# Kernel optimization log

Hardware: AMD Instinct MI355X
Metric: run time of the kernel (lower is better)

The kernel has to match this reference:

```python
import jax, jax.numpy as jnp
import numpy as np

N_NODES = 200000
N_GRAPHS = 1024
BN_EPS = 1e-5


def setup_inputs() -> dict:
    key = jax.random.key(0)
    ks = jax.random.split(key, 24)
    s = 0.05
    inp = {
        "x": jax.random.normal(ks[0], (N_NODES, 78), jnp.float32),
        "edge_index": jax.random.randint(ks[1], (2, 3200000), 0, N_NODES, jnp.int32),
        "batch": jnp.sort(jax.random.randint(ks[2], (N_NODES,), 0, N_GRAPHS, jnp.int32)),
        "target": jax.random.randint(ks[3], (N_GRAPHS, 1000), 0, 26, jnp.int32),
        "g1_w1": jax.random.normal(ks[4], (78, 32), jnp.float32) * s,
        "g1_b1": jnp.zeros((32,), jnp.float32),
        "g1_w2": jax.random.normal(ks[5], (32, 32), jnp.float32) * s,
        "g1_b2": jnp.zeros((32,), jnp.float32),
        "gW1": jax.random.normal(ks[6], (4, 32, 32), jnp.float32) * s,
        "gb1": jnp.zeros((4, 32), jnp.float32),
        "gW2": jax.random.normal(ks[7], (4, 32, 32), jnp.float32) * s,
        "gb2": jnp.zeros((4, 32), jnp.float32),
        "bn_gamma": jnp.ones((5, 32), jnp.float32),
        "bn_beta": jnp.zeros((5, 32), jnp.float32),
        "fcxd_w": jax.random.normal(ks[8], (32, 128), jnp.float32) * s,
        "fcxd_b": jnp.zeros((128,), jnp.float32),
        "embed_xt": jax.random.normal(ks[9], (26, 128), jnp.float32) * s,
        "conv_w": jax.random.normal(ks[10], (32, 1000, 8), jnp.float32) * 0.01,
        "conv_b": jnp.zeros((32,), jnp.float32),
        "fcxt_w": jax.random.normal(ks[11], (3872, 128), jnp.float32) * 0.01,
        "fcxt_b": jnp.zeros((128,), jnp.float32),
        "fc1_w": jax.random.normal(ks[12], (256, 1024), jnp.float32) * s,
        "fc1_b": jnp.zeros((1024,), jnp.float32),
        "fc2_w": jax.random.normal(ks[13], (1024, 256), jnp.float32) * s,
        "fc2_b": jnp.zeros((256,), jnp.float32),
        "out_w": jax.random.normal(ks[14], (256, 1), jnp.float32) * s,
        "out_b": jnp.zeros((1,), jnp.float32),
    }
    return inp


def _gin_layer(h, edge_index, W1, b1, W2, b2, gamma, beta):
    # GINConv (eps=0): mlp(x + sum_{j in N(i)} x_j), then ReLU then BatchNorm
    agg = jax.ops.segment_sum(h[edge_index[0]], edge_index[1], num_segments=N_NODES)
    z = h + agg
    z = jnp.maximum(z @ W1 + b1, 0.0) @ W2 + b2
    z = jnp.maximum(z, 0.0)
    mu = z.mean(axis=0)
    var = z.var(axis=0)
    return (z - mu) * jax.lax.rsqrt(var + BN_EPS) * gamma + beta


def reference(x, edge_index, batch, target,
              g1_w1, g1_b1, g1_w2, g1_b2,
              gW1, gb1, gW2, gb2, bn_gamma, bn_beta,
              fcxd_w, fcxd_b, embed_xt, conv_w, conv_b,
              fcxt_w, fcxt_b, fc1_w, fc1_b, fc2_w, fc2_b, out_w, out_b):
    # --- molecule GIN branch (dropout = identity at inference) ---
    h = _gin_layer(x, edge_index, g1_w1, g1_b1, g1_w2, g1_b2, bn_gamma[0], bn_beta[0])
    for i in range(4):
        h = _gin_layer(h, edge_index, gW1[i], gb1[i], gW2[i], gb2[i],
                       bn_gamma[i + 1], bn_beta[i + 1])
    # global add pool over graphs
    pooled = jax.ops.segment_sum(h, batch, num_segments=N_GRAPHS)  # [B,32]
    xd = jnp.maximum(pooled @ fcxd_w + fcxd_b, 0.0)                # [B,128]

    # --- protein branch: embed -> Conv1d(in_ch=seq_len=1000, k=8) -> linear ---
    e = embed_xt[target]                                            # [B,1000,128]
    conv = jax.lax.conv_general_dilated(
        e, conv_w, window_strides=(1,), padding='VALID',
        dimension_numbers=('NCH', 'OIH', 'NCH'))                    # [B,32,121]
    conv = conv + conv_b[None, :, None]
    xt = conv.reshape(conv.shape[0], -1) @ fcxt_w + fcxt_b          # [B,128]

    # --- combined dense head ---
    xc = jnp.concatenate([xd, xt], axis=1)                          # [B,256]
    xc = jnp.maximum(xc @ fc1_w + fc1_b, 0.0)
    xc = xc @ fc2_w + fc2_b
    return xc @ out_w + out_b                                       # [B,1]
```

## Files before the change

kernel.cpp:

```cpp
#include <hip/hip_runtime.h>
#include <hip/hip_fp16.h>

#define HID 32
#define BN_EPS 1e-5f
#define NBMAX 512
#define BSHIFT 9
#define SCAT_CH 8192
#define FSTRIDE 10240
#define FCAP 10240
#define DP_CH 4096

static __device__ __forceinline__ int lbound(const int* a, int n, int key) {
    int lo = 0, hi = n;
    while (lo < hi) { int m = (lo + hi) >> 1; if (a[m] < key) lo = m + 1; else hi = m; }
    return lo;
}

static __device__ __forceinline__ unsigned packh2(float a, float b) {
    __half2 h = __floats2half2_rn(a, b);
    return *reinterpret_cast<unsigned*>(&h);
}
static __device__ __forceinline__ float lo_h(unsigned v) {
    __half2 h = *reinterpret_cast<__half2*>(&v);
    return __low2float(h);
}
static __device__ __forceinline__ float hi_h(unsigned v) {
    __half2 h = *reinterpret_cast<__half2*>(&v);
    return __high2float(h);
}
static __device__ __forceinline__ float h2f(unsigned short v) {
    return __half2float(__ushort_as_half(v));
}

static __device__ __forceinline__ void addu4h(float* a, uint4 v) {
    a[0] += lo_h(v.x); a[1] += hi_h(v.x);
    a[2] += lo_h(v.y); a[3] += hi_h(v.y);
    a[4] += lo_h(v.z); a[5] += hi_h(v.z);
    a[6] += lo_h(v.w); a[7] += hi_h(v.w);
}

__global__ void __launch_bounds__(256) k_bscatter(const int* __restrict__ ei,
                                                  int* __restrict__ gcur,
                                                  int* __restrict__ pairs, int E, int NB) {
    __shared__ int h[NBMAX];
    __shared__ int lb[NBMAX];
    int t = threadIdx.x;
    int c0 = blockIdx.x * SCAT_CH;
    int end = min(c0 + SCAT_CH, E);
    for (int i = t; i < NBMAX; i += 256) h[i] = 0;
    __syncthreads();
    for (int i = c0 + t; i < end; i += 256)
        atomicAdd(&h[ei[E + i] >> BSHIFT], 1);
    __syncthreads();
    for (int b = t; b < NB; b += 256) {
        int c = h[b];
        lb[b] = c ? atomicAdd(&gcur[b], c) : 0;
        h[b] = 0;
    }
    __syncthreads();
    for (int i = c0 + t; i < end; i += 256) {
        int src = ei[i], d = ei[E + i];
        int bkt = d >> BSHIFT;
        int r = atomicAdd(&h[bkt], 1);
        pairs[bkt * FSTRIDE + lb[bkt] + r] = src | ((d & 511) << 18);
    }
}

__global__ void __launch_bounds__(512) k_bscan(const int* __restrict__ gcur,
                                               int* __restrict__ bbase,
                                               int* __restrict__ rowstart,
                                               int N, int E, int NB) {
    __shared__ int s[512];
    int t = threadIdx.x;
    int v = (t < NB) ? gcur[t] : 0;
    s[t] = v; __syncthreads();
    for (int off = 1; off < 512; off <<= 1) {
        int u = (t >= off) ? s[t - off] : 0; __syncthreads();
        s[t] += u; __syncthreads();
    }
    int excl = s[t] - v;
    if (t < NB) bbase[t] = excl;
    if (t == NB - 1) bbase[NB] = s[t];
    if (t == 0) rowstart[N] = E;
}

__global__ void __launch_bounds__(512) k_bfinal(const int* __restrict__ pairs,
                                                const int* __restrict__ bbase,
                                                const int* __restrict__ gcur,
                                                int* __restrict__ rowstart,
                                                int* __restrict__ csr, int N) {
    __shared__ int h[2048];
    __shared__ int ts[512];
    __shared__ int loc[FCAP];
    int t = threadIdx.x;
    int b = blockIdx.x;
    int base = bbase[b];
    int cnt = gcur[b];
    const int* bp = pairs + (size_t)b * FSTRIDE;
    for (int i = t; i < 2048; i += 512) h[i] = 0;
    __syncthreads();
    for (int i = t; i < cnt; i += 512) {
        int p = bp[i];
        int key = ((p >> 18) << 2) | ((p & 0x3ffff) >> 16);
        atomicAdd(&h[key], 1);
    }
    __syncthreads();
    int v0 = h[4 * t], v1 = h[4 * t + 1], v2 = h[4 * t + 2], v3 = h[4 * t + 3];
    int lsum = v0 + v1 + v2 + v3;
    ts[t] = lsum; __syncthreads();
    for (int off = 1; off < 512; off <<= 1) {
        int u = (t >= off) ? ts[t - off] : 0; __syncthreads();
        ts[t] += u; __syncthreads();
    }
    int texcl = ts[t] - lsum;
    h[4 * t]     = texcl;
    h[4 * t + 1] = texcl + v0;
    h[4 * t + 2] = texcl + v0 + v1;
    h[4 * t + 3] = texcl + v0 + v1 + v2;
    int node = b * 512 + t;
    if (node < N) rowstart[node] = base + texcl;
    __syncthreads();
    bool fit = (cnt <= FCAP);
    for (int i = t; i < cnt; i += 512) {
        int p = bp[i];
        int key = ((p >> 18) << 2) | ((p & 0x3ffff) >> 16);
        int r = atomicAdd(&h[key], 1);
        int src = p & 0x3ffff;
        if (fit) loc[r] = src; else csr[base + r] = src;
    }
    __syncthreads();
    if (fit)
        for (int i = t; i < cnt; i += 512) csr[base + i] = loc[i];
}

__global__ void __launch_bounds__(256) k_dhist(const int* __restrict__ rowstart,
                                               int* __restrict__ dh, int N) {
    __shared__ int h[512];
    int t = threadIdx.x;
    for (int i = t; i < 512; i += 256) h[i] = 0;
    __syncthreads();
    for (int i = blockIdx.x * 256 + t; i < N; i += gridDim.x * 256) {
        int d = min(rowstart[i + 1] - rowstart[i], 511);
        atomicAdd(&h[d], 1);
    }
    __syncthreads();
    for (int i = t; i < 512; i += 256)
        if (h[i]) atomicAdd(&dh[i], h[i]);
}

__global__ void __launch_bounds__(512) k_dscan(const int* __restrict__ dh,
                                               int* __restrict__ dcur) {
    __shared__ int s[512];
    int t = threadIdx.x;
    int v = dh[511 - t];
    s[t] = v; __syncthreads();
    for (int off = 1; off < 512; off <<= 1) {
        int u = (t >= off) ? s[t - off] : 0; __syncthreads();
        s[t] += u; __syncthreads();
    }
    dcur[511 - t] = s[t] - v;
}

__global__ void __launch_bounds__(256) k_dplace2(const int* __restrict__ rowstart,
                                                 int* __restrict__ dcur,
                                                 int* __restrict__ perm, int N) {
    __shared__ int h[512];
    __shared__ int base[512];
    int t = threadIdx.x;
    int c0 = blockIdx.x * DP_CH;
    int end = min(c0 + DP_CH, N);
    for (int i = t; i < 512; i += 256) h[i] = 0;
    __syncthreads();
    for (int i = c0 + t; i < end; i += 256) {
        int d = min(rowstart[i + 1] - rowstart[i], 511);
        atomicAdd(&h[d], 1);
    }
    __syncthreads();
    for (int i = t; i < 512; i += 256) {
        int c = h[i];
        base[i] = c ? atomicAdd(&dcur[i], c) : 0;
        h[i] = 0;
    }
    __syncthreads();
    for (int i = c0 + t; i < end; i += 256) {
        int d = min(rowstart[i + 1] - rowstart[i], 511);
        int r = atomicAdd(&h[d], 1);
        perm[base[d] + r] = i;
    }
}

__global__ void __launch_bounds__(256) k_A1(const float* __restrict__ x,
                                            const float* __restrict__ W,
                                            unsigned* __restrict__ Ub, int N) {
    __shared__ float xl[64 * 79];
    __shared__ float wl[78 * 33];
    int t = threadIdx.x;
    int n0 = blockIdx.x * 64;
    for (int idx = t; idx < 78 * 32; idx += 256)
        wl[(idx >> 5) * 33 + (idx & 31)] = W[idx];
    long base = (long)n0 * 78;
    for (int idx = t; idx < 64 * 78; idx += 256) {
        long g = base + idx;
        xl[(idx / 78) * 79 + (idx % 78)] = (g < (long)N * 78) ? x[g] : 0.f;
    }
    __syncthreads();
    int jp = t & 15, rg = t >> 4;
    for (int rep = 0; rep < 4; rep++) {
        int n = rg + 16 * rep;
        int node = n0 + n;
        if (node >= N) break;
        float a0 = 0.f, a1 = 0.f;
        #pragma unroll
        for (int k = 0; k < 78; k++) {
            float xv = xl[n * 79 + k];
            a0 += xv * wl[k * 33 + 2 * jp];
            a1 += xv * wl[k * 33 + 2 * jp + 1];
        }
        Ub[(size_t)node * 16 + jp] = packh2(a0, a1);
    }
}

__global__ void __launch_bounds__(256) k_BCS0(const uint4* __restrict__ Ub4,
                                              const int* __restrict__ rowstart,
                                              const int* __restrict__ csr,
                                              const int* __restrict__ perm,
                                              const float* __restrict__ b1,
                                              const float* __restrict__ W2,
                                              const float* __restrict__ b2,
                                              unsigned* __restrict__ Outb,
                                              float* __restrict__ slot, int N) {
    __shared__ float w2s[32 * 33];
    __shared__ float tl[64 * 33];
    __shared__ float redS[8][33];
    __shared__ float redQ[8][33];
    __shared__ int pl[64];
    int t = threadIdx.x;
    for (int idx = t; idx < 1024; idx += 256)
        w2s[(idx >> 5) * 33 + (idx & 31)] = W2[idx];
    if (t < 64) {
        int gid = blockIdx.x * 64 + t;
        pl[t] = (gid < N) ? perm[gid] : -1;
    }
    __syncthreads();

    int g = t >> 2, l = t & 3;
    int node = pl[g];
    bool act = (node >= 0);
    int s0 = 0, s1 = 0;
    if (act) { s0 = rowstart[node]; s1 = rowstart[node + 1]; }
    float a[8] = {0.f, 0.f, 0.f, 0.f, 0.f, 0.f, 0.f, 0.f};
    if (act) addu4h(a, Ub4[(size_t)node * 4 + l]);
    int e = s0;
    for (; e + 3 < s1; e += 4) {
        int sa = csr[e], sb = csr[e + 1], sc = csr[e + 2], sd = csr[e + 3];
        uint4 va = Ub4[(size_t)sa * 4 + l];
        uint4 vb = Ub4[(size_t)sb * 4 + l];
        uint4 vc = Ub4[(size_t)sc * 4 + l];
        uint4 vd = Ub4[(size_t)sd * 4 + l];
        addu4h(a, va); addu4h(a, vb); addu4h(a, vc); addu4h(a, vd);
    }
    for (; e < s1; e++) addu4h(a, Ub4[(size_t)csr[e] * 4 + l]);
    int f0 = 8 * l;
    #pragma unroll
    for (int i = 0; i < 8; i++)
        tl[g * 33 + f0 + i] = fmaxf(a[i] + b1[f0 + i], 0.f);
    __syncthreads();

    int j = t & 31, rg2 = t >> 5;
    float ps = 0.f, pq = 0.f;
    for (int rep = 0; rep < 8; rep++) {
        int n = rg2 + 8 * rep;
        float acc = b2[j];
        #pragma unroll
        for (int k = 0; k < 32; k++) acc += tl[n * 33 + k] * w2s[k * 33 + j];
        float xv = fmaxf(acc, 0.f);
        tl[n * 33 + j] = xv;
        if (pl[n] >= 0) { ps += xv; pq += xv * xv; }
    }
    redS[rg2][j] = ps; redQ[rg2][j] = pq;
    __syncthreads();
    if (t < 32) {
        float s = 0.f, q = 0.f;
        #pragma unroll
        for (int r = 0; r < 8; r++) { s += redS[r][t]; q += redQ[r][t]; }
        int rep = blockIdx.x & 7;
        atomicAdd(&slot[rep * 64 + t], s);
        atomicAdd(&slot[rep * 64 + 32 + t], q);
    }
    for (int idx = t; idx < 1024; idx += 256) {
        int n = idx >> 4, jp = idx & 15;
        int nod = pl[n];
        if (nod >= 0)
            Outb[(size_t)nod * 16 + jp] = packh2(tl[n * 33 + 2 * jp], tl[n * 33 + 2 * jp + 1]);
    }
}

__global__ void __launch_bounds__(256) k_BCS1(const uint4* __restrict__ Xb4,
                                              const int* __restrict__ rowstart,
                                              const int* __restrict__ csr,
                                              const int* __restrict__ perm,
                                              const float* __restrict__ pslot,
                                              const float* __restrict__ pgam,
                                              const float* __restrict__ pbet,
                                              const float* __restrict__ W1,
                                              const float* __restrict__ b1,
                                              const float* __restrict__ W2,
                                              const float* __restrict__ b2,
                                              unsigned* __restrict__ Outb,
                                              float* __restrict__ slot, int N) {
    __shared__ float w1s[32 * 33];
    __shared__ float w2s[32 * 33];
    __shared__ float zl[64 * 33];
    __shared__ float aa[32], cc[32], cw[32];
    __shared__ float dp1[64];
    __shared__ float redS[8][33];
    __shared__ float redQ[8][33];
    __shared__ int pl[64];
    int t = threadIdx.x;
    if (t < 32) {
        float s = 0.f, q = 0.f;
        #pragma unroll
        for (int r = 0; r < 8; r++) { s += pslot[r * 64 + t]; q += pslot[r * 64 + 32 + t]; }
        float mu = s / (float)N;
        float var = q / (float)N - mu * mu;
        float av = pgam[t] * rsqrtf(var + BN_EPS);
        aa[t] = av;
        cc[t] = pbet[t] - mu * av;
    }
    if (t >= 64 && t < 128) {
        int gid = blockIdx.x * 64 + (t - 64);
        pl[t - 64] = (gid < N) ? perm[gid] : -1;
    }
    __syncthreads();
    for (int idx = t; idx < 1024; idx += 256) {
        int k = idx >> 5, j = idx & 31;
        w1s[k * 33 + j] = aa[k] * W1[idx];
        w2s[k * 33 + j] = W2[idx];
    }
    if (t < 32) {
        float acc = 0.f;
        for (int k = 0; k < 32; k++) acc += cc[k] * W1[k * 32 + t];
        cw[t] = acc;
    }

    int g = t >> 2, l = t & 3;
    int node = pl[g];
    bool act = (node >= 0);
    int s0 = 0, s1 = 0;
    if (act) { s0 = rowstart[node]; s1 = rowstart[node + 1]; }
    float a[8] = {0.f, 0.f, 0.f, 0.f, 0.f, 0.f, 0.f, 0.f};
    if (act) addu4h(a, Xb4[(size_t)node * 4 + l]);
    int e = s0;
    for (; e + 3 < s1; e += 4) {
        int sa = csr[e], sb = csr[e + 1], sc = csr[e + 2], sd = csr[e + 3];
        uint4 va = Xb4[(size_t)sa * 4 + l];
        uint4 vb = Xb4[(size_t)sb * 4 + l];
        uint4 vc = Xb4[(size_t)sc * 4 + l];
        uint4 vd = Xb4[(size_t)sd * 4 + l];
        addu4h(a, va); addu4h(a, vb); addu4h(a, vc); addu4h(a, vd);
    }
    for (; e < s1; e++) addu4h(a, Xb4[(size_t)csr[e] * 4 + l]);
    int f0 = 8 * l;
    #pragma unroll
    for (int i = 0; i < 8; i++) zl[g * 33 + f0 + i] = a[i];
    if (l == 0) dp1[g] = (float)(s1 - s0 + 1);
    __syncthreads();

    int j = t & 31, rg2 = t >> 5;
    float ps = 0.f, pq = 0.f;
    for (int rep = 0; rep < 8; rep++) {
        int n = rg2 + 8 * rep;
        float acc = dp1[n] * cw[j] + b1[j];
        #pragma unroll
        for (int k = 0; k < 32; k++) acc += zl[n * 33 + k] * w1s[k * 33 + j];
        zl[n * 33 + j] = fmaxf(acc, 0.f);
        float o = b2[j];
        #pragma unroll
        for (int k = 0; k < 32; k++) o += zl[n * 33 + k] * w2s[k * 33 + j];
        float xv = fmaxf(o, 0.f);
        zl[n * 33 + j] = xv;
        if (pl[n] >= 0) { ps += xv; pq += xv * xv; }
    }
    redS[rg2][j] = ps; redQ[rg2][j] = pq;
    __syncthreads();
    if (t < 32) {
        float s = 0.f, q = 0.f;
        #pragma unroll
        for (int r = 0; r < 8; r++) { s += redS[r][t]; q += redQ[r][t]; }
        int rep = blockIdx.x & 7;
        atomicAdd(&slot[rep * 64 + t], s);
        atomicAdd(&slot[rep * 64 + 32 + t], q);
    }
    for (int idx = t; idx < 1024; idx += 256) {
        int n = idx >> 4, jp = idx & 15;
        int nod = pl[n];
        if (nod >= 0)
            Outb[(size_t)nod * 16 + jp] = packh2(zl[n * 33 + 2 * jp], zl[n * 33 + 2 * jp + 1]);
    }
}

__global__ void __launch_bounds__(128) k_pool(const unsigned short* __restrict__ Xb,
                                              const int* __restrict__ batch,
                                              const float* __restrict__ pslot,
                                              const float* __restrict__ pgam,
                                              const float* __restrict__ pbet,
                                              const float* __restrict__ fw,
                                              const float* __restrict__ fb,
                                              float* __restrict__ xc, int N) {
    __shared__ float red[4][32];
    __shared__ float pv[32];
    __shared__ float aa[32], cc[32];
    int g = blockIdx.x, t = threadIdx.x;
    if (t < 32) {
        float s = 0.f, q = 0.f;
        #pragma unroll
        for (int r = 0; r < 8; r++) { s += pslot[r * 64 + t]; q += pslot[r * 64 + 32 + t]; }
        float mu = s / (float)N;
        float var = q / (float)N - mu * mu;
        float av = pgam[t] * rsqrtf(var + BN_EPS);
        aa[t] = av;
        cc[t] = pbet[t] - mu * av;
    }
    int lo = lbound(batch, N, g);
    int hi = lbound(batch, N, g + 1);
    int j = t & 31, rs = t >> 5;
    float ps = 0.f;
    for (int i = lo + rs; i < hi; i += 4) ps += h2f(Xb[(size_t)i * 32 + j]);
    red[rs][j] = ps; __syncthreads();
    if (t < 32) {
        float s = red[0][t] + red[1][t] + red[2][t] + red[3][t];
        pv[t] = s * aa[t] + (float)(hi - lo) * cc[t];
    }
    __syncthreads();
    float acc = fb[t];
    for (int k = 0; k < 32; k++) acc += pv[k] * fw[k * 128 + t];
    xc[g * 256 + t] = fmaxf(acc, 0.f);
}

__global__ void __launch_bounds__(128) k_F2(const float* __restrict__ Emb,
                                            const float* __restrict__ fcxt,
                                            float* __restrict__ F) {
    __shared__ float er[128];
    int bid = blockIdx.x;
    int v = bid >> 5, o = bid & 31;
    int t = threadIdx.x;
    er[t] = Emb[v * 128 + t];
    __syncthreads();
    float acc[8] = {0.f, 0.f, 0.f, 0.f, 0.f, 0.f, 0.f, 0.f};
    for (int p = 0; p < 121; p++) {
        float fv = fcxt[(o * 121 + p) * 128 + t];
        #pragma unroll
        for (int k = 0; k < 8; k++) acc[k] += er[p + k] * fv;
    }
    #pragma unroll
    for (int k = 0; k < 8; k++)
        F[((size_t)v * 256 + o * 8 + k) * 128 + t] = acc[k];
}

__global__ void __launch_bounds__(128) k_cb(const float* __restrict__ fcxt,
                                            const float* __restrict__ fb,
                                            const float* __restrict__ cb,
                                            float* __restrict__ cbias) {
    int o = blockIdx.x, t = threadIdx.x;
    float acc = 0.f;
    for (int p = 0; p < 121; p++) acc += fcxt[(o * 121 + p) * 128 + t];
    float val = cb[o] * acc;
    if (o == 0) val += fb[t];
    atomicAdd(&cbias[t], val);
}

__global__ void __launch_bounds__(256) k_D2(const float* __restrict__ cw,
                                            const float* __restrict__ F,
                                            unsigned* __restrict__ Dmb) {
    __shared__ float Fl[32][128];
    __shared__ float Wl[32][64];
    int v = blockIdx.y;
    int c0 = blockIdx.x * 64;
    int t = threadIdx.x;
    int jg = t & 31, j0 = jg * 4;
    int cg = t >> 5;
    float4 acc[8];
    #pragma unroll
    for (int i = 0; i < 8; i++) acc[i] = make_float4(0.f, 0.f, 0.f, 0.f);
    for (int chunk = 0; chunk < 8; chunk++) {
        int k0 = chunk * 32;
        __syncthreads();
        for (int idx = t; idx < 4096; idx += 256) {
            int k = idx >> 7, j = idx & 127;
            Fl[k][j] = F[((size_t)v * 256 + k0 + k) * 128 + j];
        }
        for (int idx = t; idx < 2048; idx += 256) {
            int k = idx >> 6, c = idx & 63;
            int ok = k0 + k;
            Wl[k][c] = (c0 + c < 1000) ? cw[((ok >> 3) * 1000 + c0 + c) * 8 + (ok & 7)] : 0.f;
        }
        __syncthreads();
        for (int k = 0; k < 32; k++) {
            float4 fv = *(const float4*)&Fl[k][j0];
            #pragma unroll
            for (int ci = 0; ci < 8; ci++) {
                float wv = Wl[k][cg * 8 + ci];
                acc[ci].x += wv * fv.x;
                acc[ci].y += wv * fv.y;
                acc[ci].z += wv * fv.z;
                acc[ci].w += wv * fv.w;
            }
        }
    }
    #pragma unroll
    for (int ci = 0; ci < 8; ci++) {
        int c = c0 + cg * 8 + ci;
        if (c < 1000) {
            uint2 pk;
            pk.x = packh2(acc[ci].x, acc[ci].y);
            pk.y = packh2(acc[ci].z, acc[ci].w);
            *(uint2*)&Dmb[((size_t)c * 26 + v) * 64 + jg * 2] = pk;
        }
    }
}

__global__ void __launch_bounds__(256) k_xt3(const int* __restrict__ target,
                                             const uint4* __restrict__ Dm4,
                                             const float* __restrict__ cbias,
                                             float* __restrict__ xc) {
    __shared__ int tl[1000];
    __shared__ float red[16][132];
    int b = blockIdx.x, t = threadIdx.x;
    for (int i = t; i < 1000; i += 256) tl[i] = target[(size_t)b * 1000 + i];
    __syncthreads();
    int cl = t >> 4;
    int jg = t & 15;
    float acc[8] = {0.f, 0.f, 0.f, 0.f, 0.f, 0.f, 0.f, 0.f};
    for (int c = cl; c < 1000; c += 16) {
        int v = tl[c];
        uint4 d = Dm4[((size_t)c * 26 + v) * 16 + jg];
        acc[0] += lo_h(d.x); acc[1] += hi_h(d.x);
        acc[2] += lo_h(d.y); acc[3] += hi_h(d.y);
        acc[4] += lo_h(d.z); acc[5] += hi_h(d.z);
        acc[6] += lo_h(d.w); acc[7] += hi_h(d.w);
    }
    #pragma unroll
    for (int fi = 0; fi < 8; fi++) red[cl][jg * 8 + fi] = acc[fi];
    __syncthreads();
    if (t < 128) {
        float s = 0.f;
        #pragma unroll
        for (int r = 0; r < 16; r++) s += red[r][t];
        xc[(size_t)b * 256 + 128 + t] = cbias[t] + s;
    }
}

__global__ void __launch_bounds__(256) k_fc1(const float* __restrict__ xc,
                                             const float* __restrict__ w,
                                             const float* __restrict__ bias,
                                             float* __restrict__ y1) {
    __shared__ float xl[16 * 256];
    int t = threadIdx.x;
    int q0 = blockIdx.x * 256, b0 = blockIdx.y * 16;
    for (int idx = t; idx < 4096; idx += 256) xl[idx] = xc[b0 * 256 + idx];
    __syncthreads();
    int ql = t & 63, q = q0 + ql * 4;
    int bg = t >> 6;
    float4 bv = *(const float4*)&bias[q];
    float4 acc0 = bv, acc1 = bv, acc2 = bv, acc3 = bv;
    const float* xr = &xl[bg * 4 * 256];
    #pragma unroll 4
    for (int k = 0; k < 256; k++) {
        float4 wv = *(const float4*)&w[k * 1024 + q];
        float x0 = xr[k], x1 = xr[256 + k], x2 = xr[512 + k], x3 = xr[768 + k];
        acc0.x += x0 * wv.x; acc0.y += x0 * wv.y; acc0.z += x0 * wv.z; acc0.w += x0 * wv.w;
        acc1.x += x1 * wv.x; acc1.y += x1 * wv.y; acc1.z += x1 * wv.z; acc1.w += x1 * wv.w;
        acc2.x += x2 * wv.x; acc2.y += x2 * wv.y; acc2.z += x2 * wv.z; acc2.w += x2 * wv.w;
        acc3.x += x3 * wv.x; acc3.y += x3 * wv.y; acc3.z += x3 * wv.z; acc3.w += x3 * wv.w;
    }
    int b = b0 + bg * 4;
    float4 r;
    r.x = fmaxf(acc0.x, 0.f); r.y = fmaxf(acc0.y, 0.f); r.z = fmaxf(acc0.z, 0.f); r.w = fmaxf(acc0.w, 0.f);
    *(float4*)&y1[(size_t)b * 1024 + q] = r;
    r.x = fmaxf(acc1.x, 0.f); r.y = fmaxf(acc1.y, 0.f); r.z = fmaxf(acc1.z, 0.f); r.w = fmaxf(acc1.w, 0.f);
    *(float4*)&y1[(size_t)(b + 1) * 1024 + q] = r;
    r.x = fmaxf(acc2.x, 0.f); r.y = fmaxf(acc2.y, 0.f); r.z = fmaxf(acc2.z, 0.f); r.w = fmaxf(acc2.w, 0.f);
    *(float4*)&y1[(size_t)(b + 2) * 1024 + q] = r;
    r.x = fmaxf(acc3.x, 0.f); r.y = fmaxf(acc3.y, 0.f); r.z = fmaxf(acc3.z, 0.f); r.w = fmaxf(acc3.w, 0.f);
    *(float4*)&y1[(size_t)(b + 3) * 1024 + q] = r;
}

__global__ void k_wcomb(const float* __restrict__ fc2w, const float* __restrict__ fc2b,
                        const float* __restrict__ ow, const float* __restrict__ ob,
                        float* __restrict__ wc) {
    int p = blockIdx.x * 256 + threadIdx.x;
    float acc = 0.f;
    for (int q = 0; q < 256; q++) acc += fc2w[p * 256 + q] * ow[q];
    wc[p] = acc;
    if (p == 0) {
        float bc = ob[0];
        for (int q = 0; q < 256; q++) bc += fc2b[q] * ow[q];
        wc[1024] = bc;
    }
}

__global__ void __launch_bounds__(256) k_out(const float* __restrict__ y1,
                                             const float* __restrict__ wc,
                                             float* __restrict__ out) {
    __shared__ float r[256];
    int b = blockIdx.x, t = threadIdx.x;
    float acc = 0.f;
    for (int p = t; p < 1024; p += 256) acc += y1[b * 1024 + p] * wc[p];
    r[t] = acc; __syncthreads();
    for (int off = 128; off > 0; off >>= 1) {
        if (t < off) r[t] += r[t + off];
        __syncthreads();
    }
    if (t == 0) out[b] = r[0] + wc[1024];
}

extern "C" void kernel_launch(void* const* d_in, const int* in_sizes, int n_in,
                              void* d_out, int out_size, void* d_ws, size_t ws_size,
                              hipStream_t stream) {
    const float* x     = (const float*)d_in[0];
    const int*   ei    = (const int*)d_in[1];
    const int*   batch = (const int*)d_in[2];
    const int*   targ  = (const int*)d_in[3];
    const float* g1w1  = (const float*)d_in[4];
    const float* g1b1  = (const float*)d_in[5];
    const float* g1w2  = (const float*)d_in[6];
    const float* g1b2  = (const float*)d_in[7];
    const float* gW1   = (const float*)d_in[8];
    const float* gb1   = (const float*)d_in[9];
    const float* gW2   = (const float*)d_in[10];
    const float* gb2   = (const float*)d_in[11];
    const float* gam   = (const float*)d_in[12];
    const float* bet   = (const float*)d_in[13];
    const float* fcxdw = (const float*)d_in[14];
    const float* fcxdb = (const float*)d_in[15];
    const float* emb   = (const float*)d_in[16];
    const float* convw = (const float*)d_in[17];
    const float* convb = (const float*)d_in[18];
    const float* fcxtw = (const float*)d_in[19];
    const float* fcxtb = (const float*)d_in[20];
    const float* fc1w  = (const float*)d_in[21];
    const float* fc1b  = (const float*)d_in[22];
    const float* fc2w  = (const float*)d_in[23];
    const float* fc2b  = (const float*)d_in[24];
    const float* outw  = (const float*)d_in[25];
    const float* outb  = (const float*)d_in[26];

    int N = in_sizes[2];
    int E = in_sizes[1] / 2;
    int B = in_sizes[3] / 1000;
    int NB = (N + 511) >> BSHIFT;

    char* ws = (char*)d_ws;
    size_t off = 0;
    auto alloc = [&](size_t bytes) -> void* {
        void* p = ws + off;
        off += (bytes + 255) & ~(size_t)255;
        return p;
    };
    int*   rowstart = (int*)alloc((size_t)(N + 1) * 4);
    int*   bbase    = (int*)alloc((NBMAX + 1) * 4);
    int*   gcur     = (int*)alloc(NBMAX * 4);
    int*   csr      = (int*)alloc((size_t)E * 4);
    int*   perm     = (int*)alloc((size_t)N * 4);
    int*   dh       = (int*)alloc(512 * 4);
    int*   dcur     = (int*)alloc(512 * 4);
    size_t xb_bytes = (size_t)N * 64;
    size_t pairs_bytes = (size_t)NB * FSTRIDE * 4;
    char*  blk      = (char*)alloc(2 * xb_bytes > pairs_bytes ? 2 * xb_bytes : pairs_bytes);
    unsigned* XbA   = (unsigned*)blk;
    unsigned* XbB   = (unsigned*)(blk + xb_bytes);
    int*   pairs    = (int*)blk;
    unsigned* Ub    = (unsigned*)alloc((size_t)N * 16 * 4);
    float* stats    = (float*)alloc((size_t)5 * 640 * 4);
    float* xc       = (float*)alloc((size_t)B * 256 * 4);
    float* Fb       = (float*)alloc((size_t)26 * 256 * 128 * 4);
    unsigned* Dmb   = (unsigned*)alloc((size_t)1000 * 26 * 64 * 4);
    float* cbias    = (float*)alloc(128 * 4);
    float* y1       = (float*)alloc((size_t)B * 1024 * 4);
    float* wc       = (float*)alloc(1025 * 4);

    hipMemsetAsync(gcur, 0, NBMAX * 4, stream);
    hipMemsetAsync(dh, 0, 512 * 4, stream);
    hipMemsetAsync(stats, 0, (size_t)5 * 640 * 4, stream);
    hipMemsetAsync(cbias, 0, 128 * 4, stream);

    k_bscatter<<<(E + SCAT_CH - 1) / SCAT_CH, 256, 0, stream>>>(ei, gcur, pairs, E, NB);
    k_bscan<<<1, 512, 0, stream>>>(gcur, bbase, rowstart, N, E, NB);
    k_bfinal<<<NB, 512, 0, stream>>>(pairs, bbase, gcur, rowstart, csr, N);

    k_dhist<<<256, 256, 0, stream>>>(rowstart, dh, N);
    k_dscan<<<1, 512, 0, stream>>>(dh, dcur);
    k_dplace2<<<(N + DP_CH - 1) / DP_CH, 256, 0, stream>>>(rowstart, dcur, perm, N);

    int gBCS = (N + 63) / 64;

    k_A1<<<(N + 63) / 64, 256, 0, stream>>>(x, g1w1, Ub, N);
    k_BCS0<<<gBCS, 256, 0, stream>>>((const uint4*)Ub, rowstart, csr, perm,
                                     g1b1, g1w2, g1b2, XbA, stats, N);

    unsigned* bufs[2] = {XbA, XbB};
    for (int i = 0; i < 4; i++) {
        unsigned* src = bufs[i & 1];
        unsigned* dst = bufs[(i + 1) & 1];
        k_BCS1<<<gBCS, 256, 0, stream>>>((const uint4*)src, rowstart, csr, perm,
                                         stats + (size_t)i * 640, gam + i * 32, bet + i * 32,
                                         gW1 + i * 1024, gb1 + i * 32,
                                         gW2 + i * 1024, gb2 + i * 32,
                                         dst, stats + (size_t)(i + 1) * 640, N);
    }

    k_pool<<<B, 128, 0, stream>>>((const unsigned short*)XbA, batch,
                                  stats + (size_t)4 * 640, gam + 128, bet + 128,
                                  fcxdw, fcxdb, xc, N);

    k_F2<<<26 * 32, 128, 0, stream>>>(emb, fcxtw, Fb);
    k_cb<<<32, 128, 0, stream>>>(fcxtw, fcxtb, convb, cbias);
    dim3 gD(16, 26);
    k_D2<<<gD, 256, 0, stream>>>(convw, Fb, Dmb);
    k_xt3<<<B, 256, 0, stream>>>(targ, (const uint4*)Dmb, cbias, xc);

    dim3 g1(4, B / 16);
    k_fc1<<<g1, 256, 0, stream>>>(xc, fc1w, fc1b, y1);
    k_wcomb<<<4, 256, 0, stream>>>(fc2w, fc2b, outw, outb, wc);
    k_out<<<B, 256, 0, stream>>>(y1, wc, (float*)d_out);
}
```

Measured before the change: 653.8 us.

## Hoist BN weight folding into tiny kernels, shrink GIN blocks, use nontemporal gathers

BN folding and weight packing move out of each GIN block into a separate single-block kernel per layer that writes fp16-packed W1/W2 and a bias correction to global memory. The GIN kernels then read those weights directly instead of staging them in LDS. Blocks shrink from 64 to 32 nodes and 128 threads, cutting LDS use to raise occupancy, and neighbour gathers use nontemporal loads. The conv-weight kernel D2 also gets a smaller channel tile and twice as many blocks. The risks are per-k global/cache weight reads inside the matmul loops, fp16 rounding of the weights, and the nontemporal hint reducing L2 reuse of rows that many nodes share.

```diff
diff --git a/kernel.cpp b/kernel.cpp
--- a/kernel.cpp
+++ b/kernel.cpp
@@ -32,6 +32,20 @@
     return __half2float(__ushort_as_half(v));
 }
 
+static __device__ __forceinline__ uint4 ldnt4(const uint4* p) {
+#if defined(__has_builtin)
+#if __has_builtin(__builtin_nontemporal_load)
+    typedef unsigned int uv4 __attribute__((ext_vector_type(4)));
+    uv4 v = __builtin_nontemporal_load((const uv4*)p);
+    return make_uint4(v[0], v[1], v[2], v[3]);
+#else
+    return *p;
+#endif
+#else
+    return *p;
+#endif
+}
+
 static __device__ __forceinline__ void addu4h(float* a, uint4 v) {
     a[0] += lo_h(v.x); a[1] += hi_h(v.x);
     a[2] += lo_h(v.y); a[3] += hi_h(v.y);
@@ -186,6 +200,45 @@
         int d = min(rowstart[i + 1] - rowstart[i], 511);
         int r = atomicAdd(&h[d], 1);
         perm[base[d] + r] = i;
+    }
+}
+
+__global__ void k_prep0(const float* __restrict__ W2, unsigned* __restrict__ w2p) {
+    int idx = blockIdx.x * 256 + threadIdx.x;
+    if (idx < 512) {
+        int k = idx >> 4, jj = idx & 15;
+        w2p[idx] = packh2(W2[k * 32 + 2 * jj], W2[k * 32 + 2 * jj + 1]);
+    }
+}
+
+__global__ void k_fin2(const float* __restrict__ pslot, const float* __restrict__ gam,
+                       const float* __restrict__ bet, const float* __restrict__ W1,
+                       const float* __restrict__ W2, int N,
+                       unsigned* __restrict__ w1p, unsigned* __restrict__ w2p,
+                       float* __restrict__ cw32) {
+    __shared__ float aa[32], cc[32];
+    int t = threadIdx.x;
+    if (t < 32) {
+        float s = 0.f, q = 0.f;
+        #pragma unroll
+        for (int r = 0; r < 8; r++) { s += pslot[r * 64 + t]; q += pslot[r * 64 + 32 + t]; }
+        float mu = s / (float)N;
+        float var = q / (float)N - mu * mu;
+        float av = gam[t] * rsqrtf(var + BN_EPS);
+        aa[t] = av;
+        cc[t] = bet[t] - mu * av;
+    }
+    __syncthreads();
+    for (int idx = t; idx < 512; idx += 256) {
+        int k = idx >> 4, jj = idx & 15;
+        w1p[idx] = packh2(aa[k] * W1[k * 32 + 2 * jj],
+                          aa[k] * W1[k * 32 + 2 * jj + 1]);
+        w2p[idx] = packh2(W2[k * 32 + 2 * jj], W2[k * 32 + 2 * jj + 1]);
+    }
+    if (t < 32) {
+        float acc = 0.f;
+        for (int k = 0; k < 32; k++) acc += cc[k] * W1[k * 32 + t];
+        cw32[t] = acc;
     }
 }
 
@@ -220,180 +273,155 @@
     }
 }
 
-__global__ void __launch_bounds__(256) k_BCS0(const uint4* __restrict__ Ub4,
+__global__ void __launch_bounds__(128) k_BCS0(const uint4* __restrict__ Ub4,
                                               const int* __restrict__ rowstart,
                                               const int* __restrict__ csr,
                                               const int* __restrict__ perm,
                                               const float* __restrict__ b1,
-                                              const float* __restrict__ W2,
+                                              const unsigned* __restrict__ w2p,
                                               const float* __restrict__ b2,
                                               unsigned* __restrict__ Outb,
                                               float* __restrict__ slot, int N) {
-    __shared__ float w2s[32 * 33];
-    __shared__ float tl[64 * 33];
-    __shared__ float redS[8][33];
-    __shared__ float redQ[8][33];
-    __shared__ int pl[64];
-    int t = threadIdx.x;
-    for (int idx = t; idx < 1024; idx += 256)
-        w2s[(idx >> 5) * 33 + (idx & 31)] = W2[idx];
-    if (t < 64) {
-        int gid = blockIdx.x * 64 + t;
-        pl[t] = (gid < N) ? perm[gid] : -1;
-    }
-    __syncthreads();
-
+    __shared__ float zl[32 * 33];
+    __shared__ int nv[32];
+    __shared__ float redS[4][33];
+    __shared__ float redQ[4][33];
+    int t = threadIdx.x;
     int g = t >> 2, l = t & 3;
-    int node = pl[g];
+    int gid = blockIdx.x * 32 + g;
+    int node = (gid < N) ? perm[gid] : -1;
+    if (l == 0) nv[g] = node;
     bool act = (node >= 0);
     int s0 = 0, s1 = 0;
     if (act) { s0 = rowstart[node]; s1 = rowstart[node + 1]; }
     float a[8] = {0.f, 0.f, 0.f, 0.f, 0.f, 0.f, 0.f, 0.f};
-    if (act) addu4h(a, Ub4[(size_t)node * 4 + l]);
+    if (act) addu4h(a, ldnt4(Ub4 + (size_t)node * 4 + l));
     int e = s0;
     for (; e + 3 < s1; e += 4) {
         int sa = csr[e], sb = csr[e + 1], sc = csr[e + 2], sd = csr[e + 3];
-        uint4 va = Ub4[(size_t)sa * 4 + l];
-        uint4 vb = Ub4[(size_t)sb * 4 + l];
-        uint4 vc = Ub4[(size_t)sc * 4 + l];
-        uint4 vd = Ub4[(size_t)sd * 4 + l];
+        uint4 va = ldnt4(Ub4 + (size_t)sa * 4 + l);
+        uint4 vb = ldnt4(Ub4 + (size_t)sb * 4 + l);
+        uint4 vc = ldnt4(Ub4 + (size_t)sc * 4 + l);
+        uint4 vd = ldnt4(Ub4 + (size_t)sd * 4 + l);
         addu4h(a, va); addu4h(a, vb); addu4h(a, vc); addu4h(a, vd);
     }
-    for (; e < s1; e++) addu4h(a, Ub4[(size_t)csr[e] * 4 + l]);
+    for (; e < s1; e++) addu4h(a, ldnt4(Ub4 + (size_t)csr[e] * 4 + l));
     int f0 = 8 * l;
     #pragma unroll
     for (int i = 0; i < 8; i++)
-        tl[g * 33 + f0 + i] = fmaxf(a[i] + b1[f0 + i], 0.f);
+        zl[g * 33 + f0 + i] = fmaxf(a[i] + b1[f0 + i], 0.f);
     __syncthreads();
 
     int j = t & 31, rg2 = t >> 5;
+    float b2j = b2[j];
     float ps = 0.f, pq = 0.f;
     for (int rep = 0; rep < 8; rep++) {
-        int n = rg2 + 8 * rep;
-        float acc = b2[j];
+        int n = rg2 + 4 * rep;
+        float acc = b2j;
         #pragma unroll
-        for (int k = 0; k < 32; k++) acc += tl[n * 33 + k] * w2s[k * 33 + j];
+        for (int k = 0; k < 32; k++) {
+            unsigned wp = w2p[k * 16 + (j >> 1)];
+            float wv = (j & 1) ? hi_h(wp) : lo_h(wp);
+            acc += zl[n * 33 + k] * wv;
+        }
         float xv = fmaxf(acc, 0.f);
-        tl[n * 33 + j] = xv;
-        if (pl[n] >= 0) { ps += xv; pq += xv * xv; }
+        zl[n * 33 + j] = xv;
+        if (nv[n] >= 0) { ps += xv; pq += xv * xv; }
     }
     redS[rg2][j] = ps; redQ[rg2][j] = pq;
     __syncthreads();
     if (t < 32) {
-        float s = 0.f, q = 0.f;
-        #pragma unroll
-        for (int r = 0; r < 8; r++) { s += redS[r][t]; q += redQ[r][t]; }
-        int rep = blockIdx.x & 7;
-        atomicAdd(&slot[rep * 64 + t], s);
-        atomicAdd(&slot[rep * 64 + 32 + t], q);
-    }
-    for (int idx = t; idx < 1024; idx += 256) {
+        float s = redS[0][t] + redS[1][t] + redS[2][t] + redS[3][t];
+        float q = redQ[0][t] + redQ[1][t] + redQ[2][t] + redQ[3][t];
+        int rep2 = blockIdx.x & 7;
+        atomicAdd(&slot[rep2 * 64 + t], s);
+        atomicAdd(&slot[rep2 * 64 + 32 + t], q);
+    }
+    for (int idx = t; idx < 512; idx += 128) {
         int n = idx >> 4, jp = idx & 15;
-        int nod = pl[n];
+        int nod = nv[n];
         if (nod >= 0)
-            Outb[(size_t)nod * 16 + jp] = packh2(tl[n * 33 + 2 * jp], tl[n * 33 + 2 * jp + 1]);
-    }
-}
-
-__global__ void __launch_bounds__(256) k_BCS1(const uint4* __restrict__ Xb4,
+            Outb[(size_t)nod * 16 + jp] = packh2(zl[n * 33 + 2 * jp], zl[n * 33 + 2 * jp + 1]);
+    }
+}
+
+__global__ void __launch_bounds__(128) k_BCS1(const uint4* __restrict__ Xb4,
                                               const int* __restrict__ rowstart,
                                               const int* __restrict__ csr,
                                               const int* __restrict__ perm,
-                                              const float* __restrict__ pslot,
-                                              const float* __restrict__ pgam,
-                                              const float* __restrict__ pbet,
-                                              const float* __restrict__ W1,
+                                              const unsigned* __restrict__ w1p,
+                                              const unsigned* __restrict__ w2p,
+                                              const float* __restrict__ cw32,
                                               const float* __restrict__ b1,
-                                              const float* __restrict__ W2,
                                               const float* __restrict__ b2,
                                               unsigned* __restrict__ Outb,
                                               float* __restrict__ slot, int N) {
-    __shared__ float w1s[32 * 33];
-    __shared__ float w2s[32 * 33];
-    __shared__ float zl[64 * 33];
-    __shared__ float aa[32], cc[32], cw[32];
-    __shared__ float dp1[64];
-    __shared__ float redS[8][33];
-    __shared__ float redQ[8][33];
-    __shared__ int pl[64];
-    int t = threadIdx.x;
-    if (t < 32) {
-        float s = 0.f, q = 0.f;
-        #pragma unroll
-        for (int r = 0; r < 8; r++) { s += pslot[r * 64 + t]; q += pslot[r * 64 + 32 + t]; }
-        float mu = s / (float)N;
-        float var = q / (float)N - mu * mu;
-        float av = pgam[t] * rsqrtf(var + BN_EPS);
-        aa[t] = av;
-        cc[t] = pbet[t] - mu * av;
-    }
-    if (t >= 64 && t < 128) {
-        int gid = blockIdx.x * 64 + (t - 64);
-        pl[t - 64] = (gid < N) ? perm[gid] : -1;
-    }
-    __syncthreads();
-    for (int idx = t; idx < 1024; idx += 256) {
-        int k = idx >> 5, j = idx & 31;
-        w1s[k * 33 + j] = aa[k] * W1[idx];
-        w2s[k * 33 + j] = W2[idx];
-    }
-    if (t < 32) {
-        float acc = 0.f;
-        for (int k = 0; k < 32; k++) acc += cc[k] * W1[k * 32 + t];
-        cw[t] = acc;
-    }
-
+    __shared__ float zl[32 * 33];
+    __shared__ float dp1[32];
+    __shared__ int nv[32];
+    __shared__ float redS[4][33];
+    __shared__ float redQ[4][33];
+    int t = threadIdx.x;
     int g = t >> 2, l = t & 3;
-    int node = pl[g];
+    int gid = blockIdx.x * 32 + g;
+    int node = (gid < N) ? perm[gid] : -1;
     bool act = (node >= 0);
     int s0 = 0, s1 = 0;
     if (act) { s0 = rowstart[node]; s1 = rowstart[node + 1]; }
+    if (l == 0) { nv[g] = node; dp1[g] = (float)(s1 - s0 + 1); }
     float a[8] = {0.f, 0.f, 0.f, 0.f, 0.f, 0.f, 0.f, 0.f};
-    if (act) addu4h(a, Xb4[(size_t)node * 4 + l]);
+    if (act) addu4h(a, ldnt4(Xb4 + (size_t)node * 4 + l));
     int e = s0;
     for (; e + 3 < s1; e += 4) {
         int sa = csr[e], sb = csr[e + 1], sc = csr[e + 2], sd = csr[e + 3];
-        uint4 va = Xb4[(size_t)sa * 4 + l];
-        uint4 vb = Xb4[(size_t)sb * 4 + l];
-        uint4 vc = Xb4[(size_t)sc * 4 + l];
-        uint4 vd = Xb4[(size_t)sd * 4 + l];
+        uint4 va = ldnt4(Xb4 + (size_t)sa * 4 + l);
+        uint4 vb = ldnt4(Xb4 + (size_t)sb * 4 + l);
+        uint4 vc = ldnt4(Xb4 + (size_t)sc * 4 + l);
+        uint4 vd = ldnt4(Xb4 + (size_t)sd * 4 + l);
         addu4h(a, va); addu4h(a, vb); addu4h(a, vc); addu4h(a, vd);
     }
-    for (; e < s1; e++) addu4h(a, Xb4[(size_t)csr[e] * 4 + l]);
+    for (; e < s1; e++) addu4h(a, ldnt4(Xb4 + (size_t)csr[e] * 4 + l));
     int f0 = 8 * l;
     #pragma unroll
     for (int i = 0; i < 8; i++) zl[g * 33 + f0 + i] = a[i];
-    if (l == 0) dp1[g] = (float)(s1 - s0 + 1);
     __syncthreads();
 
     int j = t & 31, rg2 = t >> 5;
+    float cwj = cw32[j], b1j = b1[j], b2j = b2[j];
     float ps = 0.f, pq = 0.f;
     for (int rep = 0; rep < 8; rep++) {
-        int n = rg2 + 8 * rep;
-        float acc = dp1[n] * cw[j] + b1[j];
+        int n = rg2 + 4 * rep;
+        float acc = dp1[n] * cwj + b1j;
         #pragma unroll
-        for (int k = 0; k < 32; k++) acc += zl[n * 33 + k] * w1s[k * 33 + j];
+        for (int k = 0; k < 32; k++) {
+            unsigned wp = w1p[k * 16 + (j >> 1)];
+            float wv = (j & 1) ? hi_h(wp) : lo_h(wp);
+            acc += zl[n * 33 + k] * wv;
+        }
         zl[n * 33 + j] = fmaxf(acc, 0.f);
-        float o = b2[j];
+        float o = b2j;
         #pragma unroll
-        for (int k = 0; k < 32; k++) o += zl[n * 33 + k] * w2s[k * 33 + j];
+        for (int k = 0; k < 32; k++) {
+            unsigned wp = w2p[k * 16 + (j >> 1)];
+            float wv = (j & 1) ? hi_h(wp) : lo_h(wp);
+            o += zl[n * 33 + k] * wv;
+        }
         float xv = fmaxf(o, 0.f);
         zl[n * 33 + j] = xv;
-        if (pl[n] >= 0) { ps += xv; pq += xv * xv; }
+        if (nv[n] >= 0) { ps += xv; pq += xv * xv; }
     }
     redS[rg2][j] = ps; redQ[rg2][j] = pq;
     __syncthreads();
     if (t < 32) {
-        float s = 0.f, q = 0.f;
-        #pragma unroll
-        for (int r = 0; r < 8; r++) { s += redS[r][t]; q += redQ[r][t]; }
-        int rep = blockIdx.x & 7;
-        atomicAdd(&slot[rep * 64 + t], s);
-        atomicAdd(&slot[rep * 64 + 32 + t], q);
-    }
-    for (int idx = t; idx < 1024; idx += 256) {
+        float s = redS[0][t] + redS[1][t] + redS[2][t] + redS[3][t];
+        float q = redQ[0][t] + redQ[1][t] + redQ[2][t] + redQ[3][t];
+        int rep2 = blockIdx.x & 7;
+        atomicAdd(&slot[rep2 * 64 + t], s);
+        atomicAdd(&slot[rep2 * 64 + 32 + t], q);
+    }
+    for (int idx = t; idx < 512; idx += 128) {
         int n = idx >> 4, jp = idx & 15;
-        int nod = pl[n];
+        int nod = nv[n];
         if (nod >= 0)
             Outb[(size_t)nod * 16 + jp] = packh2(zl[n * 33 + 2 * jp], zl[n * 33 + 2 * jp + 1]);
     }
@@ -473,15 +501,15 @@
                                             const float* __restrict__ F,
                                             unsigned* __restrict__ Dmb) {
     __shared__ float Fl[32][128];
-    __shared__ float Wl[32][64];
+    __shared__ float Wl[32][33];
     int v = blockIdx.y;
-    int c0 = blockIdx.x * 64;
+    int c0 = blockIdx.x * 32;
     int t = threadIdx.x;
     int jg = t & 31, j0 = jg * 4;
     int cg = t >> 5;
-    float4 acc[8];
+    float4 acc[4];
     #pragma unroll
-    for (int i = 0; i < 8; i++) acc[i] = make_float4(0.f, 0.f, 0.f, 0.f);
+    for (int i = 0; i < 4; i++) acc[i] = make_float4(0.f, 0.f, 0.f, 0.f);
     for (int chunk = 0; chunk < 8; chunk++) {
         int k0 = chunk * 32;
         __syncthreads();
@@ -489,8 +517,8 @@
             int k = idx >> 7, j = idx & 127;
             Fl[k][j] = F[((size_t)v * 256 + k0 + k) * 128 + j];
         }
-        for (int idx = t; idx < 2048; idx += 256) {
-            int k = idx >> 6, c = idx & 63;
+        for (int idx = t; idx < 1024; idx += 256) {
+            int k = idx >> 5, c = idx & 31;
             int ok = k0 + k;
             Wl[k][c] = (c0 + c < 1000) ? cw[((ok >> 3) * 1000 + c0 + c) * 8 + (ok & 7)] : 0.f;
         }
@@ -498,8 +526,8 @@
         for (int k = 0; k < 32; k++) {
             float4 fv = *(const float4*)&Fl[k][j0];
             #pragma unroll
-            for (int ci = 0; ci < 8; ci++) {
-                float wv = Wl[k][cg * 8 + ci];
+            for (int ci = 0; ci < 4; ci++) {
+                float wv = Wl[k][cg * 4 + ci];
                 acc[ci].x += wv * fv.x;
                 acc[ci].y += wv * fv.y;
                 acc[ci].z += wv * fv.z;
@@ -508,8 +536,8 @@
         }
     }
     #pragma unroll
-    for (int ci = 0; ci < 8; ci++) {
-        int c = c0 + cg * 8 + ci;
+    for (int ci = 0; ci < 4; ci++) {
+        int c = c0 + cg * 4 + ci;
         if (c < 1000) {
             uint2 pk;
             pk.x = packh2(acc[ci].x, acc[ci].y);
@@ -664,6 +692,10 @@
     int*   perm     = (int*)alloc((size_t)N * 4);
     int*   dh       = (int*)alloc(512 * 4);
     int*   dcur     = (int*)alloc(512 * 4);
+    unsigned* w2p0  = (unsigned*)alloc(512 * 4);
+    unsigned* w1pA  = (unsigned*)alloc(4 * 512 * 4);
+    unsigned* w2pA  = (unsigned*)alloc(4 * 512 * 4);
+    float*    cwA   = (float*)alloc(4 * 32 * 4);
     size_t xb_bytes = (size_t)N * 64;
     size_t pairs_bytes = (size_t)NB * FSTRIDE * 4;
     char*  blk      = (char*)alloc(2 * xb_bytes > pairs_bytes ? 2 * xb_bytes : pairs_bytes);
@@ -692,20 +724,23 @@
     k_dscan<<<1, 512, 0, stream>>>(dh, dcur);
     k_dplace2<<<(N + DP_CH - 1) / DP_CH, 256, 0, stream>>>(rowstart, dcur, perm, N);
 
-    int gBCS = (N + 63) / 64;
-
+    int gBCS = (N + 31) / 32;
+
+    k_prep0<<<2, 256, 0, stream>>>(g1w2, w2p0);
     k_A1<<<(N + 63) / 64, 256, 0, stream>>>(x, g1w1, Ub, N);
-    k_BCS0<<<gBCS, 256, 0, stream>>>((const uint4*)Ub, rowstart, csr, perm,
-                                     g1b1, g1w2, g1b2, XbA, stats, N);
+    k_BCS0<<<gBCS, 128, 0, stream>>>((const uint4*)Ub, rowstart, csr, perm,
+                                     g1b1, w2p0, g1b2, XbA, stats, N);
 
     unsigned* bufs[2] = {XbA, XbB};
     for (int i = 0; i < 4; i++) {
         unsigned* src = bufs[i & 1];
         unsigned* dst = bufs[(i + 1) & 1];
-        k_BCS1<<<gBCS, 256, 0, stream>>>((const uint4*)src, rowstart, csr, perm,
-                                         stats + (size_t)i * 640, gam + i * 32, bet + i * 32,
-                                         gW1 + i * 1024, gb1 + i * 32,
-                                         gW2 + i * 1024, gb2 + i * 32,
+        k_fin2<<<1, 256, 0, stream>>>(stats + (size_t)i * 640, gam + i * 32, bet + i * 32,
+                                      gW1 + i * 1024, gW2 + i * 1024, N,
+                                      w1pA + i * 512, w2pA + i * 512, cwA + i * 32);
+        k_BCS1<<<gBCS, 128, 0, stream>>>((const uint4*)src, rowstart, csr, perm,
+                                         w1pA + i * 512, w2pA + i * 512, cwA + i * 32,
+                                         gb1 + i * 32, gb2 + i * 32,
                                          dst, stats + (size_t)(i + 1) * 640, N);
     }
 
@@ -715,7 +750,7 @@
 
     k_F2<<<26 * 32, 128, 0, stream>>>(emb, fcxtw, Fb);
     k_cb<<<32, 128, 0, stream>>>(fcxtw, fcxtb, convb, cbias);
-    dim3 gD(16, 26);
+    dim3 gD(32, 26);
     k_D2<<<gD, 256, 0, stream>>>(convw, Fb, Dmb);
     k_xt3<<<B, 256, 0, stream>>>(targ, (const uint4*)Dmb, cbias, xc);
 
```

Result: slower. 740.9 us (+13.3%).
